# Optimization experiments

Hardware: AMD Instinct MI355X
Metric: run time of the kernel (lower is better)

Reference implementation:

```python
import jax, jax.numpy as jnp
import numpy as np

N_DIM = 512
HEADS = 8
NUM_EXPERTS = 65536
NUM_KEYS = 256      # sqrt(NUM_EXPERTS)
DIM_KEY = 256       # N_DIM // 2
TOPK = 16           # num_experts_per_head (also product_key_topk)
SCALE = 0.02


def setup_inputs() -> dict:
    key = jax.random.key(0)
    k0, k1, k2, k3, k4 = jax.random.split(key, 5)
    x = jax.random.normal(k0, (1, 2048, N_DIM), dtype=jnp.float32)
    W_q = jax.random.normal(k1, (N_DIM, 2 * HEADS * DIM_KEY), dtype=jnp.float32) * SCALE
    keys = jax.random.normal(k2, (HEADS, NUM_KEYS, 2, DIM_KEY), dtype=jnp.float32) * SCALE
    down_embed = jax.random.normal(k3, (NUM_EXPERTS, N_DIM), dtype=jnp.float32) * SCALE
    up_embed = jax.random.normal(k4, (NUM_EXPERTS, N_DIM), dtype=jnp.float32) * SCALE
    return {"x": x, "W_q": W_q, "keys": keys, "down_embed": down_embed, "up_embed": up_embed}


def reference(x, W_q, keys, down_embed, up_embed):
    b, n, d = x.shape
    # queries: [b,n,2*h*dk] -> [2,b,n,h,dk]
    q = (x @ W_q).reshape(b, n, 2, HEADS, DIM_KEY).transpose(2, 0, 1, 3, 4)
    # similarity against product keys: [2,b,n,h,num_keys]
    sim = jnp.einsum('pbnhd,hkpd->pbnhk', q, keys)
    sx, ix = jax.lax.top_k(sim[0], TOPK)   # [b,n,h,TOPK]
    sy, iy = jax.lax.top_k(sim[1], TOPK)
    # cartesian product of the two top-k sets -> [b,n,h,TOPK*TOPK]
    all_scores = (sx[..., :, None] + sy[..., None, :]).reshape(b, n, HEADS, TOPK * TOPK)
    scores, pk_idx = jax.lax.top_k(all_scores, TOPK)  # [b,n,h,TOPK]
    # NOTE: original module indexes embeddings with pk_idx (flat top-k positions),
    # reproduced faithfully here.
    w_down = down_embed[pk_idx]  # [b,n,h,TOPK,d]
    w_up = up_embed[pk_idx]      # [b,n,h,TOPK,d]
    h = jnp.einsum('bnd,bnhkd->bnhk', x, w_down)
    h = jax.nn.gelu(h, approximate=False)
    h = jax.nn.softmax(scores, axis=-1) * h
    return jnp.einsum('bnhk,bnhkd->bnd', h, w_up)
```

## Files before the change

### kernel.cpp

```cpp
#include <hip/hip_runtime.h>
#include <math.h>

#define N_TOK 2048
#define NDIM 512
#define HEADS 8
#define TOPK 16
#define QCOLS 4096

typedef __attribute__((ext_vector_type(8))) _Float16 f16x8;
typedef __attribute__((ext_vector_type(4))) float f32x4;

__device__ __forceinline__ unsigned short f32_to_f16(float f) {
    _Float16 h = (_Float16)f;
    return __builtin_bit_cast(unsigned short, h);
}
__device__ __forceinline__ float f16_to_f32(unsigned short u) {
    return (float)__builtin_bit_cast(_Float16, u);
}
__device__ __forceinline__ void gl_lds16(const void* g, void* l) {
    __builtin_amdgcn_global_load_lds(
        (const __attribute__((address_space(1))) void*)g,
        (__attribute__((address_space(3))) void*)l, 16, 0, 0);
}

__global__ __launch_bounds__(256) void k0_prep(const float* __restrict__ x,
                                               const float* __restrict__ down,
                                               const float* __restrict__ Wq,
                                               const float* __restrict__ keys,
                                               unsigned short* __restrict__ xh,
                                               unsigned short* __restrict__ xl,
                                               unsigned short* __restrict__ Mth,
                                               unsigned short* __restrict__ Mtl) {
    const int bid = blockIdx.x;
    const int tid = threadIdx.x;
    if (bid < 256) {
        #pragma unroll
        for (int t = 0; t < 4; ++t) {
            const int i = bid * 1024 + t * 256 + tid;
            float4 v = reinterpret_cast<const float4*>(x)[i];
            float vv[4] = {v.x, v.y, v.z, v.w};
            ushort4 h, lo;
            unsigned short* hp = &h.x; unsigned short* lp = &lo.x;
            #pragma unroll
            for (int q = 0; q < 4; ++q) {
                unsigned short hh = f32_to_f16(vv[q]);
                hp[q] = hh;
                lp[q] = f32_to_f16(vv[q] - f16_to_f32(hh));
            }
            reinterpret_cast<ushort4*>(xh)[i] = h;
            reinterpret_cast<ushort4*>(xl)[i] = lo;
        }
        return;
    }
    if (bid < 512) {
        const int e = bid - 256;
        const int d0 = tid * 2;
        float2 v = *reinterpret_cast<const float2*>(&down[(size_t)e * NDIM + d0]);
        ushort2 h, lo;
        unsigned short h0 = f32_to_f16(v.x);
        unsigned short h1 = f32_to_f16(v.y);
        h.x = h0; h.y = h1;
        lo.x = f32_to_f16(v.x - f16_to_f32(h0));
        lo.y = f32_to_f16(v.y - f16_to_f32(h1));
        *reinterpret_cast<ushort2*>(&Mth[(size_t)(QCOLS + e) * NDIM + d0]) = h;
        *reinterpret_cast<ushort2*>(&Mtl[(size_t)(QCOLS + e) * NDIM + d0]) = lo;
        return;
    }
    __shared__ float As[16][64];
    __shared__ float Bs[16][64];
    const int b = bid - 512;
    const int cx = b & 7, ky = (b >> 3) & 3, ph = b >> 5;
    const int p = ph >> 3, h = ph & 7;
    const int off = p * 2048 + h * 256;
    const int c0 = cx * 64;
    const int k0 = ky * 64;
    const int lr = tid >> 2;
    const int ld4 = (tid & 3) * 4;
    const int tr = tid >> 4, tc = tid & 15;
    float acc[4][4] = {};
    const float* ap = &Wq[(size_t)(c0 + lr) * QCOLS + off + ld4];
    const float* bp = &keys[(size_t)((h * 256 + (k0 + lr)) * 2 + p) * 256 + ld4];
    float4 av = *reinterpret_cast<const float4*>(ap);
    float4 bv = *reinterpret_cast<const float4*>(bp);
    for (int d0 = 0; d0 < 256; d0 += 16) {
        __syncthreads();
        As[ld4 + 0][lr] = av.x; As[ld4 + 1][lr] = av.y; As[ld4 + 2][lr] = av.z; As[ld4 + 3][lr] = av.w;
        Bs[ld4 + 0][lr] = bv.x; Bs[ld4 + 1][lr] = bv.y; Bs[ld4 + 2][lr] = bv.z; Bs[ld4 + 3][lr] = bv.w;
        __syncthreads();
        if (d0 + 16 < 256) {
            av = *reinterpret_cast<const float4*>(ap + d0 + 16);
            bv = *reinterpret_cast<const float4*>(bp + d0 + 16);
        }
        #pragma unroll
        for (int kk = 0; kk < 16; ++kk) {
            float4 a = *reinterpret_cast<const float4*>(&As[kk][tr * 4]);
            float4 bq = *reinterpret_cast<const float4*>(&Bs[kk][tc * 4]);
            float aa[4] = {a.x, a.y, a.z, a.w}, bb[4] = {bq.x, bq.y, bq.z, bq.w};
            #pragma unroll
            for (int i = 0; i < 4; ++i)
                #pragma unroll
                for (int j = 0; j < 4; ++j) acc[i][j] += aa[i] * bb[j];
        }
    }
    #pragma unroll
    for (int j = 0; j < 4; ++j) {
        const int col = off + k0 + tc * 4 + j;
        ushort4 h4, l4;
        unsigned short* hp = &h4.x; unsigned short* lp = &l4.x;
        #pragma unroll
        for (int i = 0; i < 4; ++i) {
            float v = acc[i][j];
            unsigned short hh = f32_to_f16(v);
            hp[i] = hh;
            lp[i] = f32_to_f16(v - f16_to_f32(hh));
        }
        *reinterpret_cast<ushort4*>(&Mth[(size_t)col * NDIM + c0 + tr * 4]) = h4;
        *reinterpret_cast<ushort4*>(&Mtl[(size_t)col * NDIM + c0 + tr * 4]) = l4;
    }
}

#define BM 64
#define BN 256
#define BK 32
#define FBUF 40960
__global__ __launch_bounds__(256, 2) void kF_gemm(const unsigned short* __restrict__ xh,
                                                  const unsigned short* __restrict__ xl,
                                                  const unsigned short* __restrict__ Mth,
                                                  const unsigned short* __restrict__ Mtl,
                                                  float* __restrict__ T,
                                                  float* __restrict__ D) {
    __shared__ __align__(16) char lds[2 * FBUF];
    const int tid = threadIdx.x;
    const int w = tid >> 6, l = tid & 63;
    const int row0 = blockIdx.x * BM;
    const int g = blockIdx.y;
    const int colbase = g * 256;
    f32x4 acc[4][4] = {};

    auto stage = [&](int buf, int s) {
        const int kk = s * BK;
        char* base = lds + buf * FBUF;
        #pragma unroll
        for (int t = 0; t < 2; ++t) {
            const int q = w * 2048 + t * 1024 + l * 16;
            const int r = q >> 7;
            const int bsw = (q & 127) ^ ((r & 7) << 4);
            const unsigned short* src = (bsw < 64)
                ? xh + (size_t)(row0 + r) * NDIM + kk + (bsw >> 1)
                : xl + (size_t)(row0 + r) * NDIM + kk + ((bsw - 64) >> 1);
            gl_lds16(src, base + w * 2048 + t * 1024);
        }
        #pragma unroll
        for (int t = 0; t < 8; ++t) {
            const int q = w * 8192 + t * 1024 + l * 16;
            const int r = q >> 7;
            const int bsw = (q & 127) ^ ((r & 7) << 4);
            const unsigned short* src = (bsw < 64)
                ? Mth + (size_t)(colbase + r) * NDIM + kk + (bsw >> 1)
                : Mtl + (size_t)(colbase + r) * NDIM + kk + ((bsw - 64) >> 1);
            gl_lds16(src, base + 8192 + w * 8192 + t * 1024);
        }
    };

    stage(0, 0);
    __syncthreads();
    for (int s = 0; s < 16; ++s) {
        if (s + 1 < 16) stage((s + 1) & 1, s + 1);
        const char* base = lds + (s & 1) * FBUF;
        const int bq = (l >> 4) * 16;
        f16x8 ah[4], al[4], bh[4], bl[4];
        #pragma unroll
        for (int mi = 0; mi < 4; ++mi) {
            const int ra = mi * 16 + (l & 15);
            const int swz = (ra & 7) << 4;
            ah[mi] = *(const f16x8*)(base + ra * 128 + (bq ^ swz));
            al[mi] = *(const f16x8*)(base + ra * 128 + ((bq + 64) ^ swz));
        }
        #pragma unroll
        for (int nj = 0; nj < 4; ++nj) {
            const int rb = w * 64 + nj * 16 + (l & 15);
            const int swz = (rb & 7) << 4;
            bh[nj] = *(const f16x8*)(base + 8192 + rb * 128 + (bq ^ swz));
            bl[nj] = *(const f16x8*)(base + 8192 + rb * 128 + ((bq + 64) ^ swz));
        }
        __builtin_amdgcn_s_setprio(1);
        #pragma unroll
        for (int mi = 0; mi < 4; ++mi)
            #pragma unroll
            for (int nj = 0; nj < 4; ++nj) {
                acc[mi][nj] = __builtin_amdgcn_mfma_f32_16x16x32_f16(ah[mi], bh[nj], acc[mi][nj], 0, 0, 0);
                acc[mi][nj] = __builtin_amdgcn_mfma_f32_16x16x32_f16(ah[mi], bl[nj], acc[mi][nj], 0, 0, 0);
                acc[mi][nj] = __builtin_amdgcn_mfma_f32_16x16x32_f16(al[mi], bh[nj], acc[mi][nj], 0, 0, 0);
            }
        __builtin_amdgcn_s_setprio(0);
        __syncthreads();
    }

    if (g == 16) {
        #pragma unroll
        for (int mi = 0; mi < 4; ++mi)
            #pragma unroll
            for (int nj = 0; nj < 4; ++nj)
                #pragma unroll
                for (int r = 0; r < 4; ++r) {
                    const int row = row0 + mi * 16 + (l >> 4) * 4 + r;
                    const int col = w * 64 + nj * 16 + (l & 15);
                    D[(size_t)row * 256 + col] = acc[mi][nj][r];
                }
        return;
    }

    float* Cl = (float*)lds;
    #pragma unroll
    for (int mi = 0; mi < 4; ++mi)
        #pragma unroll
        for (int nj = 0; nj < 4; ++nj)
            #pragma unroll
            for (int r = 0; r < 4; ++r)
                Cl[(mi * 16 + (l >> 4) * 4 + r) * 260 + w * 64 + nj * 16 + (l & 15)] = acc[mi][nj][r];
    __syncthreads();

    const int grp = tid >> 4;
    const int lam = tid & 15;
    #pragma unroll
    for (int rr = 0; rr < 4; ++rr) {
        const int row = grp * 4 + rr;
        float v[16];
        #pragma unroll
        for (int j = 0; j < 16; ++j) v[j] = Cl[row * 260 + lam + 16 * j];

        #pragma unroll
        for (int k = 2; k <= 16; k <<= 1)
            #pragma unroll
            for (int j = k >> 1; j > 0; j >>= 1)
                #pragma unroll
                for (int i = 0; i < 16; ++i) {
                    const int l2 = i ^ j;
                    if (l2 > i) {
                        const bool asc = ((i & k) == 0);
                        const float lo = fminf(v[i], v[l2]), hi = fmaxf(v[i], v[l2]);
                        v[i] = asc ? lo : hi;
                        v[l2] = asc ? hi : lo;
                    }
                }
        #pragma unroll
        for (int lvl = 1; lvl <= 8; lvl <<= 1) {
            float m[16];
            #pragma unroll
            for (int q = 0; q < 16; ++q)
                m[q] = fmaxf(v[q], __shfl_xor(v[15 - q], lvl));
            #pragma unroll
            for (int j = 8; j > 0; j >>= 1)
                #pragma unroll
                for (int i = 0; i < 16; ++i) {
                    const int l2 = i ^ j;
                    if (l2 > i) {
                        const float lo = fminf(m[i], m[l2]), hi = fmaxf(m[i], m[l2]);
                        m[i] = lo; m[l2] = hi;
                    }
                }
            #pragma unroll
            for (int q = 0; q < 16; ++q) v[q] = m[q];
        }
        const int n = row0 + row;
        T[((size_t)n * 16 + g) * 16 + lam] = v[15 - lam];
    }
}

__device__ const unsigned short CAND_TBL[32] = {
    0x0100, 0x0302, 0x0504, 0x0706, 0x0908, 0x0B0A, 0x0D0C, 0x0F0E,
    0x1110, 0x1312, 0x1514, 0x1716,
    0x2120, 0x2322, 0x3024, 0x3231, 0x4033, 0x4241,
    0x5150, 0x6160, 0x7170,
    0x9080, 0xB0A0, 0xD0C0, 0xF0E0,
    0xFFFF, 0xFFFF, 0xFFFF, 0xFFFF, 0xFFFF, 0xFFFF, 0xFFFF
};

__device__ __forceinline__ float sel16(const float a[16], int i) {
    float b0 = (i & 1) ? a[1] : a[0];
    float b1 = (i & 1) ? a[3] : a[2];
    float b2 = (i & 1) ? a[5] : a[4];
    float b3 = (i & 1) ? a[7] : a[6];
    float b4 = (i & 1) ? a[9] : a[8];
    float b5 = (i & 1) ? a[11] : a[10];
    float b6 = (i & 1) ? a[13] : a[12];
    float b7 = (i & 1) ? a[15] : a[14];
    float c0 = (i & 2) ? b1 : b0;
    float c1 = (i & 2) ? b3 : b2;
    float c2 = (i & 2) ? b5 : b4;
    float c3 = (i & 2) ? b7 : b6;
    float d0 = (i & 4) ? c1 : c0;
    float d1 = (i & 4) ? c3 : c2;
    return (i & 8) ? d1 : d0;
}

__global__ __launch_bounds__(256) void kC_combine(const float* __restrict__ T,
                                                  const float* __restrict__ D,
                                                  float* __restrict__ W) {
    __shared__ unsigned long long ckey[8][50];
    __shared__ float winval[8][16];
    __shared__ int winflat[8][16];
    __shared__ int Wrow[256];

    const int tid = threadIdx.x;
    const int n = blockIdx.x;
    const int h = tid >> 5;
    const int lam = tid & 15;

    Wrow[tid] = 0;

    float sxd[16], syd[16];
    const float* t0 = &T[((size_t)n * 16 + h) * 16];
    const float* t1 = &T[((size_t)n * 16 + 8 + h) * 16];
    #pragma unroll
    for (int q = 0; q < 16; ++q) { sxd[q] = t0[q]; syd[q] = t1[q]; }

    const int lc = tid & 31;
    const unsigned int cw = CAND_TBL[lc];
    unsigned long long mykey[2]; float myval[2]; int myflat[2]; int myrank[2] = {0, 0};
    #pragma unroll
    for (int u = 0; u < 2; ++u) {
        const int fl = (cw >> (8 * u)) & 0xFF;
        const float sv = sel16(sxd, fl >> 4) + sel16(syd, fl & 15);
        const unsigned int uv = __float_as_uint(sv);
        const unsigned int mo = (uv & 0x80000000u) ? ~uv : (uv | 0x80000000u);
        mykey[u] = ((unsigned long long)mo << 8) | (unsigned long long)(255 - fl);
        myval[u] = sv; myflat[u] = fl;
        const int slot = lc * 2 + u;
        if (slot < 50) ckey[h][slot] = mykey[u];
    }
    __syncthreads();
    for (int kk = 0; kk < 50; ++kk) {
        const unsigned long long ok = ckey[h][kk];
        myrank[0] += (ok > mykey[0]) ? 1 : 0;
        myrank[1] += (ok > mykey[1]) ? 1 : 0;
    }
    #pragma unroll
    for (int u = 0; u < 2; ++u)
        if (myrank[u] < 16) { winval[h][myrank[u]] = myval[u]; winflat[h][myrank[u]] = myflat[u]; }
    __syncthreads();

    if (!(tid & 16)) {
        const float sc = winval[h][lam];
        const float m0 = winval[h][0];
        float e = expf(sc - m0);
        float esum = e;
        #pragma unroll
        for (int off = 1; off < 16; off <<= 1) esum += __shfl_xor(esum, off);
        const int fl = winflat[h][lam];
        const float hv = D[(size_t)n * 256 + fl];
        const float gg = 0.5f * hv * (1.0f + erff(hv * 0.70710678118654752f));
        const float wv = (e / esum) * gg;
        atomicAdd(&Wrow[fl], __float2int_rn(wv * 4194304.0f));
    }
    __syncthreads();
    W[(size_t)n * 256 + tid] = (float)Wrow[tid] * (1.0f / 4194304.0f);
}

__global__ __launch_bounds__(256) void k5_out(const float* __restrict__ W,
                                              const float* __restrict__ up,
                                              float* __restrict__ out) {
    __shared__ float As[16][32];
    __shared__ float Bs[16][64];
    const int row0 = blockIdx.x * 32;
    const int col0 = blockIdx.y * 64;
    const int tid = threadIdx.x;
    const int ar = tid & 31, ak = (tid >> 5) * 2;
    const int bk = tid >> 4, bc = (tid & 15) * 4;
    const int r0 = (tid >> 4) * 2, c0 = (tid & 15) * 4;
    float acc[2][4] = {};
    const float* wp = &W[(size_t)(row0 + ar) * 256 + ak];
    const float* up0 = &up[(size_t)bk * NDIM + col0 + bc];
    float2 a2 = *reinterpret_cast<const float2*>(wp);
    float4 b4 = *reinterpret_cast<const float4*>(up0);
    for (int k0 = 0; k0 < 256; k0 += 16) {
        __syncthreads();
        As[ak + 0][ar] = a2.x;
        As[ak + 1][ar] = a2.y;
        *reinterpret_cast<float4*>(&Bs[bk][bc]) = b4;
        __syncthreads();
        if (k0 + 16 < 256) {
            a2 = *reinterpret_cast<const float2*>(wp + k0 + 16);
            b4 = *reinterpret_cast<const float4*>(up0 + (size_t)16 * NDIM + (size_t)k0 * NDIM);
        }
        #pragma unroll
        for (int kk = 0; kk < 16; ++kk) {
            const float a0 = As[kk][r0], a1 = As[kk][r0 + 1];
            float4 b = *reinterpret_cast<const float4*>(&Bs[kk][c0]);
            float bb[4] = {b.x, b.y, b.z, b.w};
            #pragma unroll
            for (int j = 0; j < 4; ++j) {
                acc[0][j] += a0 * bb[j];
                acc[1][j] += a1 * bb[j];
            }
        }
    }
    #pragma unroll
    for (int i = 0; i < 2; ++i) {
        float4 o = {acc[i][0], acc[i][1], acc[i][2], acc[i][3]};
        *reinterpret_cast<float4*>(&out[(size_t)(row0 + r0 + i) * NDIM + col0 + c0]) = o;
    }
}

extern "C" void kernel_launch(void* const* d_in, const int* in_sizes, int n_in,
                              void* d_out, int out_size, void* d_ws, size_t ws_size,
                              hipStream_t stream) {
    const float* x    = (const float*)d_in[0];
    const float* Wq   = (const float*)d_in[1];
    const float* keys = (const float*)d_in[2];
    const float* down = (const float*)d_in[3];
    const float* up   = (const float*)d_in[4];
    float* out = (float*)d_out;

    char* ws = (char*)d_ws;
    unsigned short* Mth = (unsigned short*)(ws);
    unsigned short* Mtl = (unsigned short*)(ws + 4456448);
    unsigned short* xh  = (unsigned short*)(ws + 8912896);
    unsigned short* xl  = (unsigned short*)(ws + 11010048);
    float* T            = (float*)(ws + 13107200);
    float* D            = (float*)(ws + 15204352);
    float* W            = (float*)(ws + 17301504);

    k0_prep<<<1024, 256, 0, stream>>>(x, down, Wq, keys, xh, xl, Mth, Mtl);
    kF_gemm<<<dim3(32, 17), 256, 0, stream>>>(xh, xl, Mth, Mtl, T, D);
    kC_combine<<<2048, 256, 0, stream>>>(T, D, W);
    k5_out<<<dim3(64, 8), 256, 0, stream>>>(W, up, out);
}
```

Baseline: 101.9 us.

## Move Wq·keys and output GEMMs onto split-fp16 MFMA, single-buffer main GEMM

The fp32 SIMT GEMM for Wq·keys moves into its own MFMA kernel using hi/lo fp16 splits. The final W·up GEMM is also converted to MFMA, with up transposed and split in a prep kernel and W emitted as fp16 hi/lo. The main GEMM drops double buffering to a single LDS buffer with occupancy 3 and handles the epilogue in 16-row chunks to cut LDS use. This adds a launch and extra split passes over Wq and keys. It also risks losing load/compute overlap in the main GEMM.

Measured after the change: 94.20 us. 7.6% less time.

```diff
diff --git a/kernel.cpp b/kernel.cpp
--- a/kernel.cpp
+++ b/kernel.cpp
@@ -23,37 +23,60 @@
         (__attribute__((address_space(3))) void*)l, 16, 0, 0);
 }
 
-__global__ __launch_bounds__(256) void k0_prep(const float* __restrict__ x,
-                                               const float* __restrict__ down,
-                                               const float* __restrict__ Wq,
-                                               const float* __restrict__ keys,
-                                               unsigned short* __restrict__ xh,
-                                               unsigned short* __restrict__ xl,
-                                               unsigned short* __restrict__ Mth,
-                                               unsigned short* __restrict__ Mtl) {
+__device__ __forceinline__ void split_f4(const float* __restrict__ src,
+                                         unsigned short* __restrict__ dh,
+                                         unsigned short* __restrict__ dl,
+                                         int i) {
+    float4 v = reinterpret_cast<const float4*>(src)[i];
+    float vv[4] = {v.x, v.y, v.z, v.w};
+    ushort4 h, lo;
+    unsigned short* hp = &h.x; unsigned short* lp = &lo.x;
+    #pragma unroll
+    for (int q = 0; q < 4; ++q) {
+        unsigned short hh = f32_to_f16(vv[q]);
+        hp[q] = hh;
+        lp[q] = f32_to_f16(vv[q] - f16_to_f32(hh));
+    }
+    reinterpret_cast<ushort4*>(dh)[i] = h;
+    reinterpret_cast<ushort4*>(dl)[i] = lo;
+}
+
+__global__ __launch_bounds__(256) void kP_split(const float* __restrict__ x,
+                                                const float* __restrict__ Wq,
+                                                const float* __restrict__ keys,
+                                                const float* __restrict__ down,
+                                                const float* __restrict__ up,
+                                                unsigned short* __restrict__ xh,
+                                                unsigned short* __restrict__ xl,
+                                                unsigned short* __restrict__ Wqh,
+                                                unsigned short* __restrict__ Wql,
+                                                unsigned short* __restrict__ ksh,
+                                                unsigned short* __restrict__ ksl,
+                                                unsigned short* __restrict__ Mth,
+                                                unsigned short* __restrict__ Mtl,
+                                                unsigned short* __restrict__ upTh,
+                                                unsigned short* __restrict__ upTl) {
     const int bid = blockIdx.x;
     const int tid = threadIdx.x;
     if (bid < 256) {
         #pragma unroll
-        for (int t = 0; t < 4; ++t) {
-            const int i = bid * 1024 + t * 256 + tid;
-            float4 v = reinterpret_cast<const float4*>(x)[i];
-            float vv[4] = {v.x, v.y, v.z, v.w};
-            ushort4 h, lo;
-            unsigned short* hp = &h.x; unsigned short* lp = &lo.x;
-            #pragma unroll
-            for (int q = 0; q < 4; ++q) {
-                unsigned short hh = f32_to_f16(vv[q]);
-                hp[q] = hh;
-                lp[q] = f32_to_f16(vv[q] - f16_to_f32(hh));
-            }
-            reinterpret_cast<ushort4*>(xh)[i] = h;
-            reinterpret_cast<ushort4*>(xl)[i] = lo;
-        }
+        for (int t = 0; t < 4; ++t) split_f4(x, xh, xl, bid * 1024 + t * 256 + tid);
         return;
     }
-    if (bid < 512) {
-        const int e = bid - 256;
+    if (bid < 768) {
+        const int b = bid - 256;
+        #pragma unroll
+        for (int t = 0; t < 4; ++t) split_f4(Wq, Wqh, Wql, b * 1024 + t * 256 + tid);
+        return;
+    }
+    if (bid < 1024) {
+        const int b = bid - 768;
+        #pragma unroll
+        for (int t = 0; t < 4; ++t) split_f4(keys, ksh, ksl, b * 1024 + t * 256 + tid);
+        return;
+    }
+    if (bid < 1280) {
+        const int e = bid - 1024;
         const int d0 = tid * 2;
         float2 v = *reinterpret_cast<const float2*>(&down[(size_t)e * NDIM + d0]);
         ushort2 h, lo;
@@ -66,70 +89,111 @@
         *reinterpret_cast<ushort2*>(&Mtl[(size_t)(QCOLS + e) * NDIM + d0]) = lo;
         return;
     }
-    __shared__ float As[16][64];
-    __shared__ float Bs[16][64];
-    const int b = bid - 512;
-    const int cx = b & 7, ky = (b >> 3) & 3, ph = b >> 5;
+    const int b = bid - 1280;
+    #pragma unroll
+    for (int dd = 0; dd < 8; ++dd) {
+        const int d = b * 8 + dd;
+        const int e = tid;
+        const float v = up[(size_t)e * NDIM + d];
+        unsigned short hh = f32_to_f16(v);
+        upTh[(size_t)d * 256 + e] = hh;
+        upTl[(size_t)d * 256 + e] = f32_to_f16(v - f16_to_f32(hh));
+    }
+}
+
+__global__ __launch_bounds__(256) void kQ_m1(const unsigned short* __restrict__ Wqh,
+                                             const unsigned short* __restrict__ Wql,
+                                             const unsigned short* __restrict__ ksh,
+                                             const unsigned short* __restrict__ ksl,
+                                             unsigned short* __restrict__ Mth,
+                                             unsigned short* __restrict__ Mtl) {
+    __shared__ __align__(16) char lds[36864];
+    const int tid = threadIdx.x;
+    const int w = tid >> 6, l = tid & 63;
+    const int c0 = blockIdx.x * 32;
+    const int ph = blockIdx.y;
     const int p = ph >> 3, h = ph & 7;
     const int off = p * 2048 + h * 256;
-    const int c0 = cx * 64;
-    const int k0 = ky * 64;
-    const int lr = tid >> 2;
-    const int ld4 = (tid & 3) * 4;
-    const int tr = tid >> 4, tc = tid & 15;
-    float acc[4][4] = {};
-    const float* ap = &Wq[(size_t)(c0 + lr) * QCOLS + off + ld4];
-    const float* bp = &keys[(size_t)((h * 256 + (k0 + lr)) * 2 + p) * 256 + ld4];
-    float4 av = *reinterpret_cast<const float4*>(ap);
-    float4 bv = *reinterpret_cast<const float4*>(bp);
-    for (int d0 = 0; d0 < 256; d0 += 16) {
-        __syncthreads();
-        As[ld4 + 0][lr] = av.x; As[ld4 + 1][lr] = av.y; As[ld4 + 2][lr] = av.z; As[ld4 + 3][lr] = av.w;
-        Bs[ld4 + 0][lr] = bv.x; Bs[ld4 + 1][lr] = bv.y; Bs[ld4 + 2][lr] = bv.z; Bs[ld4 + 3][lr] = bv.w;
-        __syncthreads();
-        if (d0 + 16 < 256) {
-            av = *reinterpret_cast<const float4*>(ap + d0 + 16);
-            bv = *reinterpret_cast<const float4*>(bp + d0 + 16);
-        }
-        #pragma unroll
-        for (int kk = 0; kk < 16; ++kk) {
-            float4 a = *reinterpret_cast<const float4*>(&As[kk][tr * 4]);
-            float4 bq = *reinterpret_cast<const float4*>(&Bs[kk][tc * 4]);
-            float aa[4] = {a.x, a.y, a.z, a.w}, bb[4] = {bq.x, bq.y, bq.z, bq.w};
-            #pragma unroll
-            for (int i = 0; i < 4; ++i)
-                #pragma unroll
-                for (int j = 0; j < 4; ++j) acc[i][j] += aa[i] * bb[j];
-        }
-    }
-    #pragma unroll
-    for (int j = 0; j < 4; ++j) {
-        const int col = off + k0 + tc * 4 + j;
-        ushort4 h4, l4;
-        unsigned short* hp = &h4.x; unsigned short* lp = &l4.x;
-        #pragma unroll
-        for (int i = 0; i < 4; ++i) {
-            float v = acc[i][j];
-            unsigned short hh = f32_to_f16(v);
-            hp[i] = hh;
-            lp[i] = f32_to_f16(v - f16_to_f32(hh));
-        }
-        *reinterpret_cast<ushort4*>(&Mth[(size_t)col * NDIM + c0 + tr * 4]) = h4;
-        *reinterpret_cast<ushort4*>(&Mtl[(size_t)col * NDIM + c0 + tr * 4]) = l4;
-    }
+    f32x4 acc[2][4] = {};
+
+    for (int s = 0; s < 8; ++s) {
+        const int kk = s * 32;
+        __syncthreads();
+        {
+            const int q = w * 1024 + l * 16;
+            const int r = q >> 7;
+            const int bsw = (q & 127) ^ ((r & 7) << 4);
+            const unsigned short* src = (bsw < 64)
+                ? Wqh + (size_t)(c0 + r) * QCOLS + off + kk + (bsw >> 1)
+                : Wql + (size_t)(c0 + r) * QCOLS + off + kk + ((bsw - 64) >> 1);
+            gl_lds16(src, lds + w * 1024);
+        }
+        #pragma unroll
+        for (int t = 0; t < 8; ++t) {
+            const int q = w * 8192 + t * 1024 + l * 16;
+            const int r = q >> 7;
+            const int bsw = (q & 127) ^ ((r & 7) << 4);
+            const unsigned short* src = (bsw < 64)
+                ? ksh + ((size_t)(h * 256 + r) * 2 + p) * 256 + kk + (bsw >> 1)
+                : ksl + ((size_t)(h * 256 + r) * 2 + p) * 256 + kk + ((bsw - 64) >> 1);
+            gl_lds16(src, lds + 4096 + w * 8192 + t * 1024);
+        }
+        __syncthreads();
+        const int bq = (l >> 4) * 16;
+        f16x8 ah[2], al[2];
+        #pragma unroll
+        for (int mi = 0; mi < 2; ++mi) {
+            const int ra = mi * 16 + (l & 15);
+            const int swz = (ra & 7) << 4;
+            ah[mi] = *(const f16x8*)(lds + ra * 128 + (bq ^ swz));
+            al[mi] = *(const f16x8*)(lds + ra * 128 + ((bq + 64) ^ swz));
+        }
+        __builtin_amdgcn_s_setprio(1);
+        #pragma unroll
+        for (int nj = 0; nj < 4; ++nj) {
+            const int rb = w * 64 + nj * 16 + (l & 15);
+            const int swz = (rb & 7) << 4;
+            f16x8 bh = *(const f16x8*)(lds + 4096 + rb * 128 + (bq ^ swz));
+            f16x8 bl = *(const f16x8*)(lds + 4096 + rb * 128 + ((bq + 64) ^ swz));
+            #pragma unroll
+            for (int mi = 0; mi < 2; ++mi) {
+                acc[mi][nj] = __builtin_amdgcn_mfma_f32_16x16x32_f16(ah[mi], bh, acc[mi][nj], 0, 0, 0);
+                acc[mi][nj] = __builtin_amdgcn_mfma_f32_16x16x32_f16(ah[mi], bl, acc[mi][nj], 0, 0, 0);
+                acc[mi][nj] = __builtin_amdgcn_mfma_f32_16x16x32_f16(al[mi], bh, acc[mi][nj], 0, 0, 0);
+            }
+        }
+        __builtin_amdgcn_s_setprio(0);
+    }
+    #pragma unroll
+    for (int mi = 0; mi < 2; ++mi)
+        #pragma unroll
+        for (int nj = 0; nj < 4; ++nj) {
+            const int k = w * 64 + nj * 16 + (l & 15);
+            const int cb = c0 + mi * 16 + (l >> 4) * 4;
+            ushort4 h4, l4;
+            unsigned short* hp = &h4.x; unsigned short* lp = &l4.x;
+            #pragma unroll
+            for (int r = 0; r < 4; ++r) {
+                const float v = acc[mi][nj][r];
+                unsigned short hh = f32_to_f16(v);
+                hp[r] = hh;
+                lp[r] = f32_to_f16(v - f16_to_f32(hh));
+            }
+            *reinterpret_cast<ushort4*>(&Mth[(size_t)(off + k) * NDIM + cb]) = h4;
+            *reinterpret_cast<ushort4*>(&Mtl[(size_t)(off + k) * NDIM + cb]) = l4;
+        }
 }
 
 #define BM 64
 #define BN 256
 #define BK 32
-#define FBUF 40960
-__global__ __launch_bounds__(256, 2) void kF_gemm(const unsigned short* __restrict__ xh,
+__global__ __launch_bounds__(256, 3) void kF_gemm(const unsigned short* __restrict__ xh,
                                                   const unsigned short* __restrict__ xl,
                                                   const unsigned short* __restrict__ Mth,
                                                   const unsigned short* __restrict__ Mtl,
                                                   float* __restrict__ T,
                                                   float* __restrict__ D) {
-    __shared__ __align__(16) char lds[2 * FBUF];
+    __shared__ __align__(16) char lds[40960];
     const int tid = threadIdx.x;
     const int w = tid >> 6, l = tid & 63;
     const int row0 = blockIdx.x * BM;
@@ -137,9 +201,9 @@
     const int colbase = g * 256;
     f32x4 acc[4][4] = {};
 
-    auto stage = [&](int buf, int s) {
+    for (int s = 0; s < 16; ++s) {
         const int kk = s * BK;
-        char* base = lds + buf * FBUF;
+        __syncthreads();
         #pragma unroll
         for (int t = 0; t < 2; ++t) {
             const int q = w * 2048 + t * 1024 + l * 16;
@@ -148,7 +212,7 @@
             const unsigned short* src = (bsw < 64)
                 ? xh + (size_t)(row0 + r) * NDIM + kk + (bsw >> 1)
                 : xl + (size_t)(row0 + r) * NDIM + kk + ((bsw - 64) >> 1);
-            gl_lds16(src, base + w * 2048 + t * 1024);
+            gl_lds16(src, lds + w * 2048 + t * 1024);
         }
         #pragma unroll
         for (int t = 0; t < 8; ++t) {
@@ -158,43 +222,35 @@
             const unsigned short* src = (bsw < 64)
                 ? Mth + (size_t)(colbase + r) * NDIM + kk + (bsw >> 1)
                 : Mtl + (size_t)(colbase + r) * NDIM + kk + ((bsw - 64) >> 1);
-            gl_lds16(src, base + 8192 + w * 8192 + t * 1024);
-        }
-    };
-
-    stage(0, 0);
-    __syncthreads();
-    for (int s = 0; s < 16; ++s) {
-        if (s + 1 < 16) stage((s + 1) & 1, s + 1);
-        const char* base = lds + (s & 1) * FBUF;
+            gl_lds16(src, lds + 8192 + w * 8192 + t * 1024);
+        }
+        __syncthreads();
         const int bq = (l >> 4) * 16;
-        f16x8 ah[4], al[4], bh[4], bl[4];
+        f16x8 ah[4], al[4];
         #pragma unroll
         for (int mi = 0; mi < 4; ++mi) {
             const int ra = mi * 16 + (l & 15);
             const int swz = (ra & 7) << 4;
-            ah[mi] = *(const f16x8*)(base + ra * 128 + (bq ^ swz));
-            al[mi] = *(const f16x8*)(base + ra * 128 + ((bq + 64) ^ swz));
-        }
+            ah[mi] = *(const f16x8*)(lds + ra * 128 + (bq ^ swz));
+            al[mi] = *(const f16x8*)(lds + ra * 128 + ((bq + 64) ^ swz));
+        }
+        __builtin_amdgcn_s_setprio(1);
         #pragma unroll
         for (int nj = 0; nj < 4; ++nj) {
             const int rb = w * 64 + nj * 16 + (l & 15);
             const int swz = (rb & 7) << 4;
-            bh[nj] = *(const f16x8*)(base + 8192 + rb * 128 + (bq ^ swz));
-            bl[nj] = *(const f16x8*)(base + 8192 + rb * 128 + ((bq + 64) ^ swz));
-        }
-        __builtin_amdgcn_s_setprio(1);
-        #pragma unroll
-        for (int mi = 0; mi < 4; ++mi)
-            #pragma unroll
-            for (int nj = 0; nj < 4; ++nj) {
-                acc[mi][nj] = __builtin_amdgcn_mfma_f32_16x16x32_f16(ah[mi], bh[nj], acc[mi][nj], 0, 0, 0);
-                acc[mi][nj] = __builtin_amdgcn_mfma_f32_16x16x32_f16(ah[mi], bl[nj], acc[mi][nj], 0, 0, 0);
-                acc[mi][nj] = __builtin_amdgcn_mfma_f32_16x16x32_f16(al[mi], bh[nj], acc[mi][nj], 0, 0, 0);
+            f16x8 bh = *(const f16x8*)(lds + 8192 + rb * 128 + (bq ^ swz));
+            f16x8 bl = *(const f16x8*)(lds + 8192 + rb * 128 + ((bq + 64) ^ swz));
+            #pragma unroll
+            for (int mi = 0; mi < 4; ++mi) {
+                acc[mi][nj] = __builtin_amdgcn_mfma_f32_16x16x32_f16(ah[mi], bh, acc[mi][nj], 0, 0, 0);
+                acc[mi][nj] = __builtin_amdgcn_mfma_f32_16x16x32_f16(ah[mi], bl, acc[mi][nj], 0, 0, 0);
+                acc[mi][nj] = __builtin_amdgcn_mfma_f32_16x16x32_f16(al[mi], bh, acc[mi][nj], 0, 0, 0);
             }
+        }
         __builtin_amdgcn_s_setprio(0);
-        __syncthreads();
-    }
+    }
+    __syncthreads();
 
     if (g == 16) {
         #pragma unroll
@@ -211,24 +267,18 @@
     }
 
     float* Cl = (float*)lds;
-    #pragma unroll
-    for (int mi = 0; mi < 4; ++mi)
-        #pragma unroll
-        for (int nj = 0; nj < 4; ++nj)
-            #pragma unroll
-            for (int r = 0; r < 4; ++r)
-                Cl[(mi * 16 + (l >> 4) * 4 + r) * 260 + w * 64 + nj * 16 + (l & 15)] = acc[mi][nj][r];
-    __syncthreads();
-
     const int grp = tid >> 4;
     const int lam = tid & 15;
-    #pragma unroll
-    for (int rr = 0; rr < 4; ++rr) {
-        const int row = grp * 4 + rr;
+    for (int c = 0; c < 4; ++c) {
+        #pragma unroll
+        for (int nj = 0; nj < 4; ++nj)
+            #pragma unroll
+            for (int r = 0; r < 4; ++r)
+                Cl[((l >> 4) * 4 + r) * 260 + w * 64 + nj * 16 + (l & 15)] = acc[c][nj][r];
+        __syncthreads();
         float v[16];
         #pragma unroll
-        for (int j = 0; j < 16; ++j) v[j] = Cl[row * 260 + lam + 16 * j];
-
+        for (int j = 0; j < 16; ++j) v[j] = Cl[grp * 260 + lam + 16 * j];
         #pragma unroll
         for (int k = 2; k <= 16; k <<= 1)
             #pragma unroll
@@ -262,8 +312,9 @@
             #pragma unroll
             for (int q = 0; q < 16; ++q) v[q] = m[q];
         }
-        const int n = row0 + row;
+        const int n = row0 + c * 16 + grp;
         T[((size_t)n * 16 + g) * 16 + lam] = v[15 - lam];
+        __syncthreads();
     }
 }
 
@@ -296,7 +347,8 @@
 
 __global__ __launch_bounds__(256) void kC_combine(const float* __restrict__ T,
                                                   const float* __restrict__ D,
-                                                  float* __restrict__ W) {
+                                                  unsigned short* __restrict__ Wh,
+                                                  unsigned short* __restrict__ Wl) {
     __shared__ unsigned long long ckey[8][50];
     __shared__ float winval[8][16];
     __shared__ int winflat[8][16];
@@ -354,52 +406,80 @@
         atomicAdd(&Wrow[fl], __float2int_rn(wv * 4194304.0f));
     }
     __syncthreads();
-    W[(size_t)n * 256 + tid] = (float)Wrow[tid] * (1.0f / 4194304.0f);
-}
-
-__global__ __launch_bounds__(256) void k5_out(const float* __restrict__ W,
-                                              const float* __restrict__ up,
-                                              float* __restrict__ out) {
-    __shared__ float As[16][32];
-    __shared__ float Bs[16][64];
-    const int row0 = blockIdx.x * 32;
-    const int col0 = blockIdx.y * 64;
+    const float wfin = (float)Wrow[tid] * (1.0f / 4194304.0f);
+    const unsigned short hh = f32_to_f16(wfin);
+    Wh[(size_t)n * 256 + tid] = hh;
+    Wl[(size_t)n * 256 + tid] = f32_to_f16(wfin - f16_to_f32(hh));
+}
+
+__global__ __launch_bounds__(256) void k5_mfma(const unsigned short* __restrict__ Wh,
+                                               const unsigned short* __restrict__ Wl,
+                                               const unsigned short* __restrict__ upTh,
+                                               const unsigned short* __restrict__ upTl,
+                                               float* __restrict__ out) {
+    __shared__ __align__(16) char lds[20480];
     const int tid = threadIdx.x;
-    const int ar = tid & 31, ak = (tid >> 5) * 2;
-    const int bk = tid >> 4, bc = (tid & 15) * 4;
-    const int r0 = (tid >> 4) * 2, c0 = (tid & 15) * 4;
-    float acc[2][4] = {};
-    const float* wp = &W[(size_t)(row0 + ar) * 256 + ak];
-    const float* up0 = &up[(size_t)bk * NDIM + col0 + bc];
-    float2 a2 = *reinterpret_cast<const float2*>(wp);
-    float4 b4 = *reinterpret_cast<const float4*>(up0);
-    for (int k0 = 0; k0 < 256; k0 += 16) {
-        __syncthreads();
-        As[ak + 0][ar] = a2.x;
-        As[ak + 1][ar] = a2.y;
-        *reinterpret_cast<float4*>(&Bs[bk][bc]) = b4;
-        __syncthreads();
-        if (k0 + 16 < 256) {
-            a2 = *reinterpret_cast<const float2*>(wp + k0 + 16);
-            b4 = *reinterpret_cast<const float4*>(up0 + (size_t)16 * NDIM + (size_t)k0 * NDIM);
-        }
-        #pragma unroll
-        for (int kk = 0; kk < 16; ++kk) {
-            const float a0 = As[kk][r0], a1 = As[kk][r0 + 1];
-            float4 b = *reinterpret_cast<const float4*>(&Bs[kk][c0]);
-            float bb[4] = {b.x, b.y, b.z, b.w};
-            #pragma unroll
-            for (int j = 0; j < 4; ++j) {
-                acc[0][j] += a0 * bb[j];
-                acc[1][j] += a1 * bb[j];
+    const int w = tid >> 6, l = tid & 63;
+    const int n0 = blockIdx.x * 32;
+    const int d0 = blockIdx.y * 128;
+    f32x4 acc[2][2] = {};
+
+    for (int s = 0; s < 8; ++s) {
+        const int kk = s * 32;
+        __syncthreads();
+        {
+            const int q = w * 1024 + l * 16;
+            const int r = q >> 7;
+            const int bsw = (q & 127) ^ ((r & 7) << 4);
+            const unsigned short* src = (bsw < 64)
+                ? Wh + (size_t)(n0 + r) * 256 + kk + (bsw >> 1)
+                : Wl + (size_t)(n0 + r) * 256 + kk + ((bsw - 64) >> 1);
+            gl_lds16(src, lds + w * 1024);
+        }
+        #pragma unroll
+        for (int t = 0; t < 4; ++t) {
+            const int q = w * 4096 + t * 1024 + l * 16;
+            const int r = q >> 7;
+            const int bsw = (q & 127) ^ ((r & 7) << 4);
+            const unsigned short* src = (bsw < 64)
+                ? upTh + (size_t)(d0 + r) * 256 + kk + (bsw >> 1)
+                : upTl + (size_t)(d0 + r) * 256 + kk + ((bsw - 64) >> 1);
+            gl_lds16(src, lds + 4096 + w * 4096 + t * 1024);
+        }
+        __syncthreads();
+        const int bq = (l >> 4) * 16;
+        f16x8 ah[2], al[2];
+        #pragma unroll
+        for (int mi = 0; mi < 2; ++mi) {
+            const int ra = mi * 16 + (l & 15);
+            const int swz = (ra & 7) << 4;
+            ah[mi] = *(const f16x8*)(lds + ra * 128 + (bq ^ swz));
+            al[mi] = *(const f16x8*)(lds + ra * 128 + ((bq + 64) ^ swz));
+        }
+        #pragma unroll
+        for (int nj = 0; nj < 2; ++nj) {
+            const int rb = w * 32 + nj * 16 + (l & 15);
+            const int swz = (rb & 7) << 4;
+            f16x8 bh = *(const f16x8*)(lds + 4096 + rb * 128 + (bq ^ swz));
+            f16x8 bl = *(const f16x8*)(lds + 4096 + rb * 128 + ((bq + 64) ^ swz));
+            #pragma unroll
+            for (int mi = 0; mi < 2; ++mi) {
+                acc[mi][nj] = __builtin_amdgcn_mfma_f32_16x16x32_f16(ah[mi], bh, acc[mi][nj], 0, 0, 0);
+                acc[mi][nj] = __builtin_amdgcn_mfma_f32_16x16x32_f16(ah[mi], bl, acc[mi][nj], 0, 0, 0);
+                acc[mi][nj] = __builtin_amdgcn_mfma_f32_16x16x32_f16(al[mi], bh, acc[mi][nj], 0, 0, 0);
             }
         }
     }
     #pragma unroll
-    for (int i = 0; i < 2; ++i) {
-        float4 o = {acc[i][0], acc[i][1], acc[i][2], acc[i][3]};
-        *reinterpret_cast<float4*>(&out[(size_t)(row0 + r0 + i) * NDIM + col0 + c0]) = o;
-    }
+    for (int mi = 0; mi < 2; ++mi)
+        #pragma unroll
+        for (int nj = 0; nj < 2; ++nj)
+            #pragma unroll
+            for (int r = 0; r < 4; ++r) {
+                const int row = n0 + mi * 16 + (l >> 4) * 4 + r;
+                const int col = d0 + w * 32 + nj * 16 + (l & 15);
+                out[(size_t)row * NDIM + col] = acc[mi][nj][r];
+            }
 }
 
 extern "C" void kernel_launch(void* const* d_in, const int* in_sizes, int n_in,
@@ -413,16 +493,25 @@
     float* out = (float*)d_out;
 
     char* ws = (char*)d_ws;
-    unsigned short* Mth = (unsigned short*)(ws);
-    unsigned short* Mtl = (unsigned short*)(ws + 4456448);
-    unsigned short* xh  = (unsigned short*)(ws + 8912896);
-    unsigned short* xl  = (unsigned short*)(ws + 11010048);
-    float* T            = (float*)(ws + 13107200);
-    float* D            = (float*)(ws + 15204352);
-    float* W            = (float*)(ws + 17301504);
-
-    k0_prep<<<1024, 256, 0, stream>>>(x, down, Wq, keys, xh, xl, Mth, Mtl);
+    unsigned short* Mth  = (unsigned short*)(ws);
+    unsigned short* Mtl  = (unsigned short*)(ws + 4456448);
+    unsigned short* xh   = (unsigned short*)(ws + 8912896);
+    unsigned short* xl   = (unsigned short*)(ws + 11010048);
+    unsigned short* Wqh  = (unsigned short*)(ws + 13107200);
+    unsigned short* Wql  = (unsigned short*)(ws + 17301504);
+    unsigned short* ksh  = (unsigned short*)(ws + 21495808);
+    unsigned short* ksl  = (unsigned short*)(ws + 23592960);
+    unsigned short* upTh = (unsigned short*)(ws + 25690112);
+    unsigned short* upTl = (unsigned short*)(ws + 25952256);
+    float* T             = (float*)(ws + 26214400);
+    float* D             = (float*)(ws + 28311552);
+    unsigned short* Wh   = (unsigned short*)(ws + 30408704);
+    unsigned short* Wl   = (unsigned short*)(ws + 31457280);
+
+    kP_split<<<1344, 256, 0, stream>>>(x, Wq, keys, down, up,
+                                       xh, xl, Wqh, Wql, ksh, ksl, Mth, Mtl, upTh, upTl);
+    kQ_m1<<<dim3(16, 16), 256, 0, stream>>>(Wqh, Wql, ksh, ksl, Mth, Mtl);
     kF_gemm<<<dim3(32, 17), 256, 0, stream>>>(xh, xl, Mth, Mtl, T, D);
-    kC_combine<<<2048, 256, 0, stream>>>(T, D, W);
-    k5_out<<<dim3(64, 8), 256, 0, stream>>>(W, up, out);
-}
+    kC_combine<<<2048, 256, 0, stream>>>(T, D, Wh, Wl);
+    k5_mfma<<<dim3(64, 4), 256, 0, stream>>>(Wh, Wl, upTh, upTl, out);
+}
```
